# Kernel tuning notes

Hardware: AMD Instinct MI355X
Metric: run time of the kernel (lower is better)

The kernel has to match this reference:

```python
import math
import jax, jax.numpy as jnp
import numpy as np


def setup_inputs() -> dict:
    key = jax.random.key(0)
    ks = jax.random.split(key, 6)
    b, t, e, h = 4, 1024, 512, 8
    x = jax.random.normal(ks[0], (b, t, e), dtype=jnp.float32)
    s = 0.02  # small init scale to keep logits sane
    Wq = jax.random.normal(ks[1], (e, e * h), dtype=jnp.float32) * s
    Wk = jax.random.normal(ks[2], (e, e * h), dtype=jnp.float32) * s
    Wv = jax.random.normal(ks[3], (e, e * h), dtype=jnp.float32) * s
    Wo = jax.random.normal(ks[4], (e * h, e), dtype=jnp.float32) * s
    bo = jnp.zeros((e,), dtype=jnp.float32)
    return {"x": x, "Wq": Wq, "Wk": Wk, "Wv": Wv, "Wo": Wo, "bo": bo}


def reference(x, Wq, Wk, Wv, Wo, bo):
    b, t, e = x.shape
    h = Wq.shape[1] // e  # wide attention: each head uses full emb dim
    # project and split heads -> (b, h, t, e)
    q = (x @ Wq).reshape(b, t, h, e).transpose(0, 2, 1, 3)
    k = (x @ Wk).reshape(b, t, h, e).transpose(0, 2, 1, 3)
    v = (x @ Wv).reshape(b, t, h, e).transpose(0, 2, 1, 3)
    q = q / math.sqrt(e)
    dot = jnp.einsum("bhqe,bhke->bhqk", q, k)  # (b, h, t, t)
    # causal mask: positions j > i get -inf (mask_diagonal=False -> offset=1)
    causal = jnp.tril(jnp.ones((t, t), dtype=bool))
    dot = jnp.where(causal[None, None], dot, -jnp.inf)
    att = jax.nn.softmax(dot, axis=-1)
    out = jnp.einsum("bhqk,bhke->bhqe", att, v)
    out = out.transpose(0, 2, 1, 3).reshape(b, t, h * e)
    return out @ Wo + bo
```

## Files before the change

### kernel.cpp

```cpp
#include <hip/hip_runtime.h>
#include <hip/hip_bf16.h>

typedef unsigned short u16;
typedef __attribute__((ext_vector_type(4))) float f32x4;
typedef __attribute__((ext_vector_type(8))) short s16x8;
typedef __attribute__((ext_vector_type(4))) short s16x4;

#define DEVFN static __device__ __forceinline__

DEVFN u16 f2bf(float f) {
  unsigned u = __float_as_uint(f);
  return (u16)((u + 0x7fffu + ((u >> 16) & 1u)) >> 16);
}
DEVFN float bf2f(u16 h) { return __uint_as_float(((unsigned)h) << 16); }

DEVFN void gl_lds16(const void* g, void* l) {
  __builtin_amdgcn_global_load_lds(
      (const __attribute__((address_space(1))) unsigned int*)g,
      (__attribute__((address_space(3))) unsigned int*)l, 16, 0, 0);
}

DEVFN f32x4 mfma16(s16x8 a, s16x8 b, f32x4 c) {
  return __builtin_amdgcn_mfma_f32_16x16x32_bf16(a, b, c, 0, 0, 0);
}

__global__ void k_cvt4(const float4* __restrict__ x, const float4* __restrict__ Wq,
                       const float4* __restrict__ Wk, const float4* __restrict__ Wv,
                       u16* __restrict__ dst, float qscale, int n4) {
  const int z = blockIdx.y;
  const float4* src = (z == 0) ? x : (z == 1) ? Wq : (z == 2) ? Wk : Wv;
  const float scale = (z == 1) ? qscale : 1.f;
  u16* d = (z == 0) ? dst : dst + 2097152 + (size_t)z * 2097152;
  int i = blockIdx.x * 256 + threadIdx.x;
  if (i >= n4) return;
  float4 v = src[i];
  s16x4 o;
  o[0] = (short)f2bf(v.x * scale); o[1] = (short)f2bf(v.y * scale);
  o[2] = (short)f2bf(v.z * scale); o[3] = (short)f2bf(v.w * scale);
  *(s16x4*)(d + (size_t)i * 4) = o;
}

__global__ void k_transpose_w(const float* __restrict__ src, u16* __restrict__ dst,
                              int K, int N) {
  __shared__ float tile[64][65];
  int k0 = blockIdx.x * 64, n0 = blockIdx.y * 64;
  int t = threadIdx.x, c = t & 63, r4 = t >> 6;
#pragma unroll
  for (int i = 0; i < 16; ++i) {
    int r = i * 4 + r4;
    tile[r][c] = src[(size_t)(k0 + r) * N + n0 + c];
  }
  __syncthreads();
#pragma unroll
  for (int i = 0; i < 16; ++i) {
    int r = i * 4 + r4;
    dst[(size_t)(n0 + r) * K + k0 + c] = f2bf(tile[c][r]);
  }
}

__global__ void k_transpose_x(const u16* __restrict__ xb, u16* __restrict__ xT) {
  __shared__ u16 tile[64][65];
  const int bz = blockIdx.z;
  const int r0 = blockIdx.x * 64, c0 = blockIdx.y * 64;
  int t = threadIdx.x, c = t & 63, r4 = t >> 6;
#pragma unroll
  for (int i = 0; i < 16; ++i) {
    int r = i * 4 + r4;
    tile[r][c] = xb[(size_t)(bz * 1024 + r0 + r) * 512 + c0 + c];
  }
  __syncthreads();
#pragma unroll
  for (int i = 0; i < 16; ++i) {
    int r = i * 4 + r4;
    xT[(size_t)bz * 524288 + (size_t)(c0 + r) * 1024 + r0 + c] = tile[c][r];
  }
}

template <int BM, int BN, int EPI, int CAUSAL, int VARK>
__global__ void __launch_bounds__(256) k_gemm(
    const u16* __restrict__ A, const u16* __restrict__ Bt,
    void* __restrict__ Cp, const float* __restrict__ bias,
    int K, int lda, int ldb, int ldc,
    size_t sAb, size_t sAh, size_t sBb, size_t sBh, size_t sCb, size_t sCh) {
  const unsigned nx = gridDim.x, ny = gridDim.y;
  const unsigned nwg = nx * ny * gridDim.z;
  const unsigned L = blockIdx.x + nx * (blockIdx.y + ny * blockIdx.z);
  const unsigned o = (nwg & 7) ? L : ((L & 7) * (nwg >> 3) + (L >> 3));
  const unsigned bx = o % nx, o2 = o / nx;
  const unsigned by = o2 % ny, bz = o2 / ny;

  if (CAUSAL && bx > by) return;
  constexpr int MR = BM / 32, NR = BN / 32;
  constexpr int LPT = (BM + BN) / 64;
  constexpr int ABUF = BM * 32, BBUF = BN * 32;
  __shared__ alignas(16) u16 Alds[3 * ABUF];
  __shared__ alignas(16) u16 Blds[3 * BBUF];
  const int tid = threadIdx.x, lane = tid & 63, wv = tid >> 6;
  const int wr = wv >> 1, wc = wv & 1;
  const int row0 = by * BM, col0 = bx * BN;
  const int zb = bz >> 3, zh = bz & 7;
  const char* Ab = (const char*)(A + (size_t)zb * sAb + (size_t)zh * sAh);
  const char* Bb = (const char*)(Bt + (size_t)zb * sBb + (size_t)zh * sBh);
  const size_t coff = (size_t)zb * sCb + (size_t)zh * sCh;
  const int Klim = VARK ? (by + 1) * BM : K;
  const int ntiles = Klim >> 5;
  const f32x4 zero4 = {0.f, 0.f, 0.f, 0.f};

  const int scb = (((lane & 3) ^ ((lane >> 3) & 3))) * 16;
  auto stage = [&](int buf, int k0) {
    char* abase = (char*)(Alds + buf * ABUF);
    char* bbase = (char*)(Blds + buf * BBUF);
#pragma unroll
    for (int j = 0; j < BM / 64; ++j) {
      int ch = j * 4 + wv;
      int r = ch * 16 + (lane >> 2);
      gl_lds16(Ab + ((size_t)(row0 + r) * lda + k0) * 2 + scb, abase + ch * 1024);
    }
#pragma unroll
    for (int j = 0; j < BN / 64; ++j) {
      int ch = j * 4 + wv;
      int r = ch * 16 + (lane >> 2);
      gl_lds16(Bb + ((size_t)(col0 + r) * ldb + k0) * 2 + scb, bbase + ch * 1024);
    }
  };

  f32x4 acc[MR][NR];
#pragma unroll
  for (int m = 0; m < MR; ++m)
#pragma unroll
    for (int n = 0; n < NR; ++n) acc[m][n] = zero4;

  stage(0, 0);
  if (ntiles > 1) stage(1, 32);

  const int rcb = (((lane >> 4) ^ ((lane >> 1) & 3)) & 3) * 16;

  int t = 0;
  for (int k0 = 0; k0 < Klim; k0 += 32, ++t) {
    if (t + 1 < ntiles)
      asm volatile("s_waitcnt vmcnt(%0)" :: "i"(LPT) : "memory");
    else
      asm volatile("s_waitcnt vmcnt(0)" ::: "memory");
    __builtin_amdgcn_s_barrier();
    asm volatile("" ::: "memory");
    if (t + 2 < ntiles) stage((t + 2) % 3, k0 + 64);
    const char* abase = (const char*)(Alds + (t % 3) * ABUF);
    const char* bbase = (const char*)(Blds + (t % 3) * BBUF);
    s16x8 af[MR], bfr[NR];
#pragma unroll
    for (int m = 0; m < MR; ++m)
      af[m] = *(const s16x8*)(abase +
               (wr * (BM / 2) + m * 16 + (lane & 15)) * 64 + rcb);
#pragma unroll
    for (int n = 0; n < NR; ++n)
      bfr[n] = *(const s16x8*)(bbase +
                (wc * (BN / 2) + n * 16 + (lane & 15)) * 64 + rcb);
    __builtin_amdgcn_s_setprio(1);
#pragma unroll
    for (int m = 0; m < MR; ++m)
#pragma unroll
      for (int n = 0; n < NR; ++n) acc[m][n] = mfma16(af[m], bfr[n], acc[m][n]);
    __builtin_amdgcn_s_setprio(0);
  }
#pragma unroll
  for (int m = 0; m < MR; ++m)
#pragma unroll
    for (int n = 0; n < NR; ++n)
#pragma unroll
      for (int i = 0; i < 4; ++i) {
        int r = row0 + wr * (BM / 2) + m * 16 + (lane >> 4) * 4 + i;
        int c = col0 + wc * (BN / 2) + n * 16 + (lane & 15);
        if (EPI == 0)
          ((u16*)Cp)[coff + (size_t)r * ldc + c] = f2bf(acc[m][n][i]);
        else if (EPI == 1)
          ((float*)Cp)[coff + (size_t)r * ldc + c] = acc[m][n][i] + bias[c];
        else
          ((float*)Cp)[coff + (size_t)r * ldc + c] = acc[m][n][i];
      }
}

__global__ void __launch_bounds__(256) k_softmax(u16* __restrict__ S) {
  const int tid = threadIdx.x, lane = tid & 63, w = tid >> 6;
  const int row = blockIdx.x * 4 + w;
  const int q = row & 1023;
  u16* rowp = S + (size_t)(row >> 10) * 1048576 + (size_t)q * 1024;
  const int c0 = lane * 8, c1 = 512 + lane * 8;
  const bool hi = (q >= 512);
  s16x8 v0 = *(const s16x8*)(rowp + c0);
  s16x8 v1 = {};
  if (hi) v1 = *(const s16x8*)(rowp + c1);
  float f[16];
#pragma unroll
  for (int j = 0; j < 8; ++j) {
    f[j]     = (c0 + j <= q)       ? bf2f((u16)v0[j]) : -3e38f;
    f[8 + j] = (hi && c1 + j <= q) ? bf2f((u16)v1[j]) : -3e38f;
  }
  float m = f[0];
#pragma unroll
  for (int j = 1; j < 16; ++j) m = fmaxf(m, f[j]);
  m = fmaxf(m, __shfl_xor(m, 1));
  m = fmaxf(m, __shfl_xor(m, 2));
  m = fmaxf(m, __shfl_xor(m, 4));
  m = fmaxf(m, __shfl_xor(m, 8));
  m = fmaxf(m, __shfl_xor(m, 16));
  m = fmaxf(m, __shfl_xor(m, 32));
  float sum = 0.f;
#pragma unroll
  for (int j = 0; j < 16; ++j) { f[j] = __expf(f[j] - m); sum += f[j]; }
  sum += __shfl_xor(sum, 1);
  sum += __shfl_xor(sum, 2);
  sum += __shfl_xor(sum, 4);
  sum += __shfl_xor(sum, 8);
  sum += __shfl_xor(sum, 16);
  sum += __shfl_xor(sum, 32);
  const float inv = 1.f / sum;
#pragma unroll
  for (int j = 0; j < 8; ++j) {
    v0[j] = (short)f2bf(f[j] * inv);
    v1[j] = (short)f2bf(f[8 + j] * inv);
  }
  *(s16x8*)(rowp + c0) = v0;
  if (hi) *(s16x8*)(rowp + c1) = v1;
}

__global__ void k_reduce2(const float4* __restrict__ P, const float4* __restrict__ bias,
                          float4* __restrict__ out, int n4) {
  int i = blockIdx.x * 256 + threadIdx.x;
  if (i >= n4) return;
  float4 a = P[i], b = P[i + 524288];
  float4 bb = bias[i & 127];
  float4 o;
  o.x = a.x + b.x + bb.x;
  o.y = a.y + b.y + bb.y;
  o.z = a.z + b.z + bb.z;
  o.w = a.w + b.w + bb.w;
  out[i] = o;
}

extern "C" void kernel_launch(void* const* d_in, const int* in_sizes, int n_in,
                              void* d_out, int out_size, void* d_ws, size_t ws_size,
                              hipStream_t stream) {
  (void)in_sizes; (void)n_in; (void)out_size; (void)ws_size;
  const float* x  = (const float*)d_in[0];
  const float* Wq = (const float*)d_in[1];
  const float* Wk = (const float*)d_in[2];
  const float* Wv = (const float*)d_in[3];
  const float* Wo = (const float*)d_in[4];
  const float* bo = (const float*)d_in[5];
  float* out = (float*)d_out;

  u16* ws   = (u16*)d_ws;
  u16* xb   = ws;
  u16* xT   = ws + 2097152;
  u16* Wqb  = ws + 4194304;
  u16* Wkb  = ws + 6291456;
  u16* Wvb  = ws + 8388608;
  u16* WoT  = ws + 10485760;
  u16* G    = ws + 12582912;
  u16* WvoT = ws + 14680064;
  u16* y    = ws + 16777216;
  u16* S    = ws + 33554432;
  u16* Z    = ws + 67108864;
  float* Pp = (float*)(ws + 16777216);

  const float qscale = 0.044194173824159216f;

  k_cvt4<<<dim3(2048, 4), 256, 0, stream>>>((const float4*)x, (const float4*)Wq,
                                            (const float4*)Wk, (const float4*)Wv,
                                            ws, qscale, 524288);
  k_transpose_w<<<dim3(64, 8), 256, 0, stream>>>(Wo, WoT, 4096, 512);
  k_transpose_x<<<dim3(16, 8, 4), 256, 0, stream>>>(xb, xT);

  k_gemm<64, 64, 0, 0, 0><<<dim3(8, 8, 8), 256, 0, stream>>>(
      Wkb, Wqb, (void*)G, nullptr, 512, 4096, 4096, 512,
      0, 512, 0, 512, 0, 262144);
  k_gemm<64, 64, 0, 0, 0><<<dim3(8, 8, 8), 256, 0, stream>>>(
      WoT, Wvb, (void*)WvoT, nullptr, 512, 4096, 4096, 4096,
      0, 512, 0, 512, 0, 512);

  k_gemm<128, 128, 0, 0, 0><<<dim3(4, 32, 8), 256, 0, stream>>>(
      xb, G, (void*)y, nullptr, 512, 512, 512, 512,
      0, 0, 0, 262144, 0, 2097152);

  k_gemm<128, 128, 0, 1, 0><<<dim3(8, 8, 32), 256, 0, stream>>>(
      y, xb, (void*)S, nullptr, 512, 512, 512, 1024,
      524288, 2097152, 524288, 0, 8388608, 1048576);

  k_softmax<<<8192, 256, 0, stream>>>(S);

  k_gemm<128, 128, 0, 0, 1><<<dim3(4, 8, 32), 256, 0, stream>>>(
      S, xT, (void*)Z, nullptr, 1024, 1024, 1024, 4096,
      8388608, 1048576, 524288, 0, 4194304, 512);

  k_gemm<128, 64, 2, 0, 0><<<dim3(8, 32, 2), 256, 0, stream>>>(
      Z, WvoT, (void*)Pp, nullptr, 2048, 4096, 4096, 512,
      0, 2048, 0, 2048, 0, 2097152);
  k_reduce2<<<2048, 256, 0, stream>>>((const float4*)Pp, (const float4*)bo,
                                      (float4*)out, 524288);
}
```

Measured before the change: 193.6 us.

## Use 256x128 eight-wave GEMM tiles, fuse prep kernels, split final GEMM K eightfold

Replaces the templated GEMM with a single 256x128-tile, 512-thread kernel, with 8 waves each computing a 64x64 sub-tile. Staging loads are distributed across the waves, and the causal skip and variable-K limits are adapted to the larger row tile. The three preprocessing kernels are merged into one launch, and x is now transposed directly from fp32. The output projection is split eight ways over K, with a reduction that sums eight partials plus bias. The aim is to cut launch count and raise per-tile reuse, at the cost of fewer workgroups for the small GEMMs, more causal waste per tile, and extra partial-sum traffic.

Result: no change. 191.6 us (-1.0%).

```diff
diff --git a/kernel.cpp b/kernel.cpp
--- a/kernel.cpp
+++ b/kernel.cpp
@@ -24,64 +24,67 @@
   return __builtin_amdgcn_mfma_f32_16x16x32_bf16(a, b, c, 0, 0, 0);
 }
 
-__global__ void k_cvt4(const float4* __restrict__ x, const float4* __restrict__ Wq,
-                       const float4* __restrict__ Wk, const float4* __restrict__ Wv,
-                       u16* __restrict__ dst, float qscale, int n4) {
-  const int z = blockIdx.y;
-  const float4* src = (z == 0) ? x : (z == 1) ? Wq : (z == 2) ? Wk : Wv;
-  const float scale = (z == 1) ? qscale : 1.f;
-  u16* d = (z == 0) ? dst : dst + 2097152 + (size_t)z * 2097152;
-  int i = blockIdx.x * 256 + threadIdx.x;
-  if (i >= n4) return;
-  float4 v = src[i];
-  s16x4 o;
-  o[0] = (short)f2bf(v.x * scale); o[1] = (short)f2bf(v.y * scale);
-  o[2] = (short)f2bf(v.z * scale); o[3] = (short)f2bf(v.w * scale);
-  *(s16x4*)(d + (size_t)i * 4) = o;
-}
-
-__global__ void k_transpose_w(const float* __restrict__ src, u16* __restrict__ dst,
-                              int K, int N) {
+__global__ void k_prep(const float* __restrict__ x, const float* __restrict__ Wq,
+                       const float* __restrict__ Wk, const float* __restrict__ Wv,
+                       const float* __restrict__ Wo, u16* __restrict__ ws,
+                       float qscale) {
   __shared__ float tile[64][65];
-  int k0 = blockIdx.x * 64, n0 = blockIdx.y * 64;
-  int t = threadIdx.x, c = t & 63, r4 = t >> 6;
-#pragma unroll
-  for (int i = 0; i < 16; ++i) {
-    int r = i * 4 + r4;
-    tile[r][c] = src[(size_t)(k0 + r) * N + n0 + c];
-  }
-  __syncthreads();
-#pragma unroll
-  for (int i = 0; i < 16; ++i) {
-    int r = i * 4 + r4;
-    dst[(size_t)(n0 + r) * K + k0 + c] = f2bf(tile[c][r]);
-  }
-}
-
-__global__ void k_transpose_x(const u16* __restrict__ xb, u16* __restrict__ xT) {
-  __shared__ u16 tile[64][65];
-  const int bz = blockIdx.z;
-  const int r0 = blockIdx.x * 64, c0 = blockIdx.y * 64;
-  int t = threadIdx.x, c = t & 63, r4 = t >> 6;
-#pragma unroll
-  for (int i = 0; i < 16; ++i) {
-    int r = i * 4 + r4;
-    tile[r][c] = xb[(size_t)(bz * 1024 + r0 + r) * 512 + c0 + c];
-  }
-  __syncthreads();
-#pragma unroll
-  for (int i = 0; i < 16; ++i) {
-    int r = i * 4 + r4;
-    xT[(size_t)bz * 524288 + (size_t)(c0 + r) * 1024 + r0 + c] = tile[c][r];
-  }
-}
-
-template <int BM, int BN, int EPI, int CAUSAL, int VARK>
-__global__ void __launch_bounds__(256) k_gemm(
+  const int z = blockIdx.y, bid = blockIdx.x, tid = threadIdx.x;
+  if (z < 4) {
+    const float4* src = (z == 0) ? (const float4*)x : (z == 1) ? (const float4*)Wq
+                      : (z == 2) ? (const float4*)Wk : (const float4*)Wv;
+    const float scale = (z == 1) ? qscale : 1.f;
+    u16* d = (z == 0) ? ws : ws + 2097152 + (size_t)z * 2097152;
+    int i = bid * 256 + tid;
+    float4 v = src[i];
+    s16x4 o;
+    o[0] = (short)f2bf(v.x * scale); o[1] = (short)f2bf(v.y * scale);
+    o[2] = (short)f2bf(v.z * scale); o[3] = (short)f2bf(v.w * scale);
+    *(s16x4*)(d + (size_t)i * 4) = o;
+    return;
+  }
+  if (bid >= 512) return;
+  const int c = tid & 63, r4 = tid >> 6;
+  if (z == 4) {
+    const int k0 = (bid & 63) * 64, n0 = (bid >> 6) * 64;
+    u16* WoT = ws + 10485760;
+#pragma unroll
+    for (int i = 0; i < 16; ++i) {
+      int r = i * 4 + r4;
+      tile[r][c] = Wo[(size_t)(k0 + r) * 512 + n0 + c];
+    }
+    __syncthreads();
+#pragma unroll
+    for (int i = 0; i < 16; ++i) {
+      int r = i * 4 + r4;
+      WoT[(size_t)(n0 + r) * 4096 + k0 + c] = f2bf(tile[c][r]);
+    }
+  } else {
+    const int bz = bid >> 7, r0 = (bid & 15) * 64, c0 = ((bid >> 4) & 7) * 64;
+    u16* xT = ws + 2097152;
+#pragma unroll
+    for (int i = 0; i < 16; ++i) {
+      int r = i * 4 + r4;
+      tile[r][c] = x[(size_t)(bz * 1024 + r0 + r) * 512 + c0 + c];
+    }
+    __syncthreads();
+#pragma unroll
+    for (int i = 0; i < 16; ++i) {
+      int r = i * 4 + r4;
+      xT[(size_t)bz * 524288 + (size_t)(c0 + r) * 1024 + r0 + c] = f2bf(tile[c][r]);
+    }
+  }
+}
+
+template <int EPI, int CAUSAL, int VARK>
+__global__ void __launch_bounds__(512, 2) k_gemm2(
     const u16* __restrict__ A, const u16* __restrict__ Bt,
     void* __restrict__ Cp, const float* __restrict__ bias,
     int K, int lda, int ldb, int ldc,
     size_t sAb, size_t sAh, size_t sBb, size_t sBh, size_t sCb, size_t sCh) {
+  constexpr int BM = 256, BN = 128, MR = 4, NR = 4;
+  constexpr int LPT = 3;
+  constexpr int ABUF = BM * 32, BBUF = BN * 32;
   const unsigned nx = gridDim.x, ny = gridDim.y;
   const unsigned nwg = nx * ny * gridDim.z;
   const unsigned L = blockIdx.x + nx * (blockIdx.y + ny * blockIdx.z);
@@ -89,20 +92,17 @@
   const unsigned bx = o % nx, o2 = o / nx;
   const unsigned by = o2 % ny, bz = o2 / ny;
 
-  if (CAUSAL && bx > by) return;
-  constexpr int MR = BM / 32, NR = BN / 32;
-  constexpr int LPT = (BM + BN) / 64;
-  constexpr int ABUF = BM * 32, BBUF = BN * 32;
+  const int row0 = by * BM, col0 = bx * BN;
+  if (CAUSAL && col0 >= row0 + BM) return;
   __shared__ alignas(16) u16 Alds[3 * ABUF];
   __shared__ alignas(16) u16 Blds[3 * BBUF];
   const int tid = threadIdx.x, lane = tid & 63, wv = tid >> 6;
   const int wr = wv >> 1, wc = wv & 1;
-  const int row0 = by * BM, col0 = bx * BN;
   const int zb = bz >> 3, zh = bz & 7;
   const char* Ab = (const char*)(A + (size_t)zb * sAb + (size_t)zh * sAh);
   const char* Bb = (const char*)(Bt + (size_t)zb * sBb + (size_t)zh * sBh);
   const size_t coff = (size_t)zb * sCb + (size_t)zh * sCh;
-  const int Klim = VARK ? (by + 1) * BM : K;
+  const int Klim = VARK ? (row0 + BM) : K;
   const int ntiles = Klim >> 5;
   const f32x4 zero4 = {0.f, 0.f, 0.f, 0.f};
 
@@ -111,16 +111,16 @@
     char* abase = (char*)(Alds + buf * ABUF);
     char* bbase = (char*)(Blds + buf * BBUF);
 #pragma unroll
-    for (int j = 0; j < BM / 64; ++j) {
-      int ch = j * 4 + wv;
-      int r = ch * 16 + (lane >> 2);
-      gl_lds16(Ab + ((size_t)(row0 + r) * lda + k0) * 2 + scb, abase + ch * 1024);
-    }
-#pragma unroll
-    for (int j = 0; j < BN / 64; ++j) {
-      int ch = j * 4 + wv;
-      int r = ch * 16 + (lane >> 2);
-      gl_lds16(Bb + ((size_t)(col0 + r) * ldb + k0) * 2 + scb, bbase + ch * 1024);
+    for (int j = 0; j < 3; ++j) {
+      int ch = wv * 3 + j;
+      if (ch < 16) {
+        int r = ch * 16 + (lane >> 2);
+        gl_lds16(Ab + ((size_t)(row0 + r) * lda + k0) * 2 + scb, abase + ch * 1024);
+      } else {
+        int r = (ch - 16) * 16 + (lane >> 2);
+        gl_lds16(Bb + ((size_t)(col0 + r) * ldb + k0) * 2 + scb,
+                 bbase + (ch - 16) * 1024);
+      }
     }
   };
 
@@ -150,11 +150,11 @@
 #pragma unroll
     for (int m = 0; m < MR; ++m)
       af[m] = *(const s16x8*)(abase +
-               (wr * (BM / 2) + m * 16 + (lane & 15)) * 64 + rcb);
+               (wr * 64 + m * 16 + (lane & 15)) * 64 + rcb);
 #pragma unroll
     for (int n = 0; n < NR; ++n)
       bfr[n] = *(const s16x8*)(bbase +
-                (wc * (BN / 2) + n * 16 + (lane & 15)) * 64 + rcb);
+                (wc * 64 + n * 16 + (lane & 15)) * 64 + rcb);
     __builtin_amdgcn_s_setprio(1);
 #pragma unroll
     for (int m = 0; m < MR; ++m)
@@ -168,8 +168,8 @@
     for (int n = 0; n < NR; ++n)
 #pragma unroll
       for (int i = 0; i < 4; ++i) {
-        int r = row0 + wr * (BM / 2) + m * 16 + (lane >> 4) * 4 + i;
-        int c = col0 + wc * (BN / 2) + n * 16 + (lane & 15);
+        int r = row0 + wr * 64 + m * 16 + (lane >> 4) * 4 + i;
+        int c = col0 + wc * 64 + n * 16 + (lane & 15);
         if (EPI == 0)
           ((u16*)Cp)[coff + (size_t)r * ldc + c] = f2bf(acc[m][n][i]);
         else if (EPI == 1)
@@ -223,18 +223,20 @@
   if (hi) *(s16x8*)(rowp + c1) = v1;
 }
 
-__global__ void k_reduce2(const float4* __restrict__ P, const float4* __restrict__ bias,
+__global__ void k_reduce8(const float4* __restrict__ P, const float4* __restrict__ bias,
                           float4* __restrict__ out, int n4) {
   int i = blockIdx.x * 256 + threadIdx.x;
   if (i >= n4) return;
-  float4 a = P[i], b = P[i + 524288];
   float4 bb = bias[i & 127];
-  float4 o;
-  o.x = a.x + b.x + bb.x;
-  o.y = a.y + b.y + bb.y;
-  o.z = a.z + b.z + bb.z;
-  o.w = a.w + b.w + bb.w;
-  out[i] = o;
+  float sx = bb.x, sy = bb.y, sz = bb.z, sw = bb.w;
+#pragma unroll
+  for (int j = 0; j < 8; ++j) {
+    float4 a = P[i + (size_t)j * 524288];
+    sx += a.x; sy += a.y; sz += a.z; sw += a.w;
+  }
+  float4 o2;
+  o2.x = sx; o2.y = sy; o2.z = sz; o2.w = sw;
+  out[i] = o2;
 }
 
 extern "C" void kernel_launch(void* const* d_in, const int* in_sizes, int n_in,
@@ -261,40 +263,36 @@
   u16* y    = ws + 16777216;
   u16* S    = ws + 33554432;
   u16* Z    = ws + 67108864;
-  float* Pp = (float*)(ws + 16777216);
+  float* Pp = (float*)(ws + 33554432);
 
   const float qscale = 0.044194173824159216f;
 
-  k_cvt4<<<dim3(2048, 4), 256, 0, stream>>>((const float4*)x, (const float4*)Wq,
-                                            (const float4*)Wk, (const float4*)Wv,
-                                            ws, qscale, 524288);
-  k_transpose_w<<<dim3(64, 8), 256, 0, stream>>>(Wo, WoT, 4096, 512);
-  k_transpose_x<<<dim3(16, 8, 4), 256, 0, stream>>>(xb, xT);
-
-  k_gemm<64, 64, 0, 0, 0><<<dim3(8, 8, 8), 256, 0, stream>>>(
+  k_prep<<<dim3(2048, 6), 256, 0, stream>>>(x, Wq, Wk, Wv, Wo, ws, qscale);
+
+  k_gemm2<0, 0, 0><<<dim3(4, 2, 8), 512, 0, stream>>>(
       Wkb, Wqb, (void*)G, nullptr, 512, 4096, 4096, 512,
       0, 512, 0, 512, 0, 262144);
-  k_gemm<64, 64, 0, 0, 0><<<dim3(8, 8, 8), 256, 0, stream>>>(
+  k_gemm2<0, 0, 0><<<dim3(4, 2, 8), 512, 0, stream>>>(
       WoT, Wvb, (void*)WvoT, nullptr, 512, 4096, 4096, 4096,
       0, 512, 0, 512, 0, 512);
 
-  k_gemm<128, 128, 0, 0, 0><<<dim3(4, 32, 8), 256, 0, stream>>>(
+  k_gemm2<0, 0, 0><<<dim3(4, 16, 8), 512, 0, stream>>>(
       xb, G, (void*)y, nullptr, 512, 512, 512, 512,
       0, 0, 0, 262144, 0, 2097152);
 
-  k_gemm<128, 128, 0, 1, 0><<<dim3(8, 8, 32), 256, 0, stream>>>(
+  k_gemm2<0, 1, 0><<<dim3(8, 4, 32), 512, 0, stream>>>(
       y, xb, (void*)S, nullptr, 512, 512, 512, 1024,
       524288, 2097152, 524288, 0, 8388608, 1048576);
 
   k_softmax<<<8192, 256, 0, stream>>>(S);
 
-  k_gemm<128, 128, 0, 0, 1><<<dim3(4, 8, 32), 256, 0, stream>>>(
+  k_gemm2<0, 0, 1><<<dim3(4, 4, 32), 512, 0, stream>>>(
       S, xT, (void*)Z, nullptr, 1024, 1024, 1024, 4096,
       8388608, 1048576, 524288, 0, 4194304, 512);
 
-  k_gemm<128, 64, 2, 0, 0><<<dim3(8, 32, 2), 256, 0, stream>>>(
-      Z, WvoT, (void*)Pp, nullptr, 2048, 4096, 4096, 512,
-      0, 2048, 0, 2048, 0, 2097152);
-  k_reduce2<<<2048, 256, 0, stream>>>((const float4*)Pp, (const float4*)bo,
+  k_gemm2<2, 0, 0><<<dim3(4, 16, 8), 512, 0, stream>>>(
+      Z, WvoT, (void*)Pp, nullptr, 512, 4096, 4096, 512,
+      0, 512, 0, 512, 0, 2097152);
+  k_reduce8<<<2048, 256, 0, stream>>>((const float4*)Pp, (const float4*)bo,
                                       (float4*)out, 524288);
 }
```
